# Optimization experiments

Measured on AMD Instinct MI355X. Metric: run time of the kernel, lower is better.

Reference implementation:

```python
import jax, jax.numpy as jnp
import numpy as np

D = 128      # d_model
H = 8        # n_heads
HD = D // H  # head_dim = 16
E = 256      # n_experts
R = 32       # kv_lora_rank
B, T = 4, 512
EPS = 1e-6


def _dense_init(k, fi, fo):
    s = float(1.0 / np.sqrt(fi))
    return jax.random.uniform(k, (fi, fo), minval=-s, maxval=s, dtype=jnp.float32)


def setup_inputs() -> dict:
    key = jax.random.key(0)
    ks = jax.random.split(key, 16)
    rng = np.random.RandomState(42)
    Q, _ = np.linalg.qr(rng.randn(D, D))
    glim = float(np.sqrt(6.0 / (D + D)))
    return {
        'x': jax.random.normal(ks[0], (B, T, D), dtype=jnp.float32),
        'g1': jnp.ones((D,), jnp.float32),
        'qW': _dense_init(ks[1], D, D), 'qb': jnp.zeros((D,), jnp.float32),
        'kdW': _dense_init(ks[2], D, R), 'kdb': jnp.zeros((R,), jnp.float32),
        'kuW': _dense_init(ks[3], R, 2 * D), 'kub': jnp.zeros((2 * D,), jnp.float32),
        'oW': _dense_init(ks[4], D, D), 'ob': jnp.zeros((D,), jnp.float32),
        'rot': jnp.asarray(Q, jnp.float32),
        'tq_scale': jnp.ones((D,), jnp.float32),
        's1W': _dense_init(ks[5], D, D), 's1b': jnp.zeros((D,), jnp.float32),
        's2W': _dense_init(ks[6], D, D), 's2b': jnp.zeros((D,), jnp.float32),
        'g2': jnp.ones((D,), jnp.float32),
        'gateW': _dense_init(ks[7], D, E), 'gateb': jnp.zeros((E,), jnp.float32),
        'expW': jax.random.uniform(ks[8], (E, D, D), minval=-glim, maxval=glim, dtype=jnp.float32),
        'm1W': _dense_init(ks[9], D, D), 'm1b': jnp.zeros((D,), jnp.float32),
        'm2W': _dense_init(ks[10], D, D), 'm2b': jnp.zeros((D,), jnp.float32),
    }


def _rmsnorm(x, g):
    return g * (x / jnp.sqrt(jnp.mean(x * x, axis=-1, keepdims=True) + EPS))


def _swiglu(x, w1, b1, w2, b2):
    gate = x @ w1 + b1
    return gate * jax.nn.sigmoid(gate) * (x @ w2 + b2)


def _mla(x, qW, qb, kdW, kdb, kuW, kub, oW, ob):
    b, t = x.shape[0], x.shape[1]
    q = (x @ qW + qb).reshape(b, t, H, HD)
    kv = ((x @ kdW + kdb) @ kuW + kub).reshape(b, t, H, 2 * HD)
    k, v = jnp.split(kv, 2, axis=-1)
    q = jax.nn.elu(q) + 1.0
    k = jax.nn.elu(k) + 1.0
    # linear attention: context[b,h,d,e] = sum_t k[b,t,h,d] v[b,t,h,e]
    context = jnp.einsum('bthd,bthe->bhde', k, v)
    out = jnp.einsum('bthd,bhde->bthe', q, context)
    k_sum = jnp.sum(k, axis=1)  # [b,h,d]
    z = 1.0 / (jnp.einsum('bthd,bhd->bth', q, k_sum) + EPS)
    out = out * z[..., None]
    return out.reshape(b, t, D) @ oW + ob


def _turbo_quant(x, rot, scale):
    x = x @ rot
    mag = jnp.sqrt(jnp.mean(x * x, axis=-1, keepdims=True) + EPS)
    phase = x / mag
    qp = jnp.clip(phase * 127.0, -127.0, 127.0) / 127.0
    phase = jax.lax.stop_gradient(qp - phase) + phase  # straight-through
    return phase * mag * scale


def _moe(h, gateW, gateb, expW, m1W, m1b, m2W, m2b):
    gate_scores = jax.nn.softmax(h @ gateW + gateb, axis=-1)  # [B,T,E]
    top_vals, top_idx = jax.lax.top_k(gate_scores, 2)
    top_w = top_vals / (jnp.sum(top_vals, axis=-1, keepdims=True) + EPS)
    # dense all-expert compute as in the original module
    eo = jnp.einsum('btd,edo->bteo', h, expW)  # [B,T,E,D]
    mask = jnp.sum(jax.nn.one_hot(top_idx, E, dtype=h.dtype) * top_w[..., None], axis=2)  # [B,T,E]
    wavg = jnp.einsum('bteo,bte->bto', eo, mask)
    wavg = _swiglu(wavg, m1W, m1b, m2W, m2b)
    diff_sq = jnp.square(eo - wavg[:, :, None, :])
    wvar = jnp.einsum('bteo,bte->bto', diff_sq, mask)
    consensus = jnp.exp(-jnp.mean(wvar, axis=-1))  # [B,T]
    return wavg, consensus


def reference(x, g1, qW, qb, kdW, kdb, kuW, kub, oW, ob, rot, tq_scale,
              s1W, s1b, s2W, s2b, g2, gateW, gateb, expW, m1W, m1b, m2W, m2b):
    attn_out = _turbo_quant(_mla(_rmsnorm(x, g1), qW, qb, kdW, kdb, kuW, kub, oW, ob), rot, tq_scale)
    x = x + _swiglu(attn_out, s1W, s1b, s2W, s2b)
    moe_out, consensus = _moe(_rmsnorm(x, g2), gateW, gateb, expW, m1W, m1b, m2W, m2b)
    return x + moe_out, consensus
```

## Files before the change

kernel.cpp:

```cpp
#include <hip/hip_runtime.h>
#include <hip/hip_bf16.h>
#include <math.h>

static constexpr int Dd   = 128;
static constexpr int NH   = 8;
static constexpr int HD   = 16;
static constexpr int NE   = 256;
static constexpr int RR   = 32;
static constexpr int BB   = 4;
static constexpr int TT   = 512;
static constexpr int NTOK = BB * TT;
static constexpr int TPB  = 4;
static constexpr int SLOTS = 256;
#define EPSF 1e-6f

__device__ __forceinline__ float elu1(float v) { return v > 0.f ? v + 1.f : expf(v); }
__device__ __forceinline__ float sigm(float v) { return 1.f / (1.f + expf(-v)); }

__global__ __launch_bounds__(256) void k_init(
    const float* __restrict__ oW, const float* __restrict__ ob,
    const float* __restrict__ rot,
    const float* __restrict__ kdW, const float* __restrict__ kdb,
    const float* __restrict__ kuW, const float* __restrict__ kub,
    float* __restrict__ oR, float* __restrict__ bR,
    float* __restrict__ kvW, float* __restrict__ bkv,
    float* __restrict__ ctx, float* __restrict__ ksum, int* __restrict__ cnt) {
  const int blk = blockIdx.x, tid = threadIdx.x;
  if (blk < 64) {
    int row = blk * 2 + (tid >> 7), col = tid & 127;
    const float* ow = oW + row * 128;
    float acc = 0.f;
#pragma unroll 8
    for (int k = 0; k < 128; k++) acc += ow[k] * rot[k * 128 + col];
    oR[row * 128 + col] = acc;
  } else if (blk == 64) {
    if (tid < 128) {
      float acc = 0.f;
#pragma unroll 8
      for (int k = 0; k < 128; k++) acc += ob[k] * rot[k * 128 + tid];
      bR[tid] = acc;
    }
    {
      float acc = kub[tid];
#pragma unroll
      for (int k = 0; k < 32; k++) acc += kdb[k] * kuW[k * 256 + tid];
      bkv[tid] = acc;
    }
    for (int i = tid; i < 32 * 256; i += 256) ctx[i] = 0.f;
    for (int i = tid; i < 512; i += 256) ksum[i] = 0.f;
    cnt[tid] = 0;
  } else {
    int idx = (blk - 65) * 256 + tid;
    int row = idx >> 8, col = idx & 255;
    const float* kw = kdW + row * 32;
    float acc = 0.f;
#pragma unroll
    for (int k = 0; k < 32; k++) acc += kw[k] * kuW[k * 256 + col];
    kvW[row * 256 + col] = acc;
  }
}

__global__ __launch_bounds__(768) void k_pre(
    const float* __restrict__ x, const float* __restrict__ g1,
    const float* __restrict__ qW, const float* __restrict__ qb,
    const float* __restrict__ kvW, const float* __restrict__ bkv,
    float* __restrict__ qbuf, float* __restrict__ kvbuf) {
  const int tid = threadIdx.x;
  const int lane = tid & 63;
  const int n0 = blockIdx.x * TPB;

  __shared__ float4 xgT[128];
  __shared__ float4 qpart[128];
  __shared__ float4 kvpart[256];
  __shared__ float4 rtmp[2];

  if (tid < 128) {
    int j = tid;
    float g1j = g1[j];
    float v[4], xg[4];
#pragma unroll
    for (int t = 0; t < 4; t++) {
      float xv = x[(n0 + t) * Dd + j];
      v[t] = xv * xv;
      xg[t] = xv * g1j;
    }
    xgT[j] = make_float4(xg[0], xg[1], xg[2], xg[3]);
#pragma unroll
    for (int o = 32; o > 0; o >>= 1) {
#pragma unroll
      for (int t = 0; t < 4; t++) v[t] += __shfl_xor(v[t], o, 64);
    }
    if (lane == 0) rtmp[tid >> 6] = make_float4(v[0], v[1], v[2], v[3]);
  }
  __syncthreads();

  float a0 = 0, a1 = 0, a2 = 0, a3 = 0;
  const bool isq = tid < 256;
  int j, kh;
  if (isq) {
    j = tid & 127; kh = tid >> 7;
    const float* Wp = qW + (kh * 64) * Dd + j;
    const float4* hb = xgT + kh * 64;
#pragma unroll 16
    for (int i = 0; i < 64; i++) {
      float4 h4 = hb[i];
      float w = Wp[i * Dd];
      a0 += h4.x * w; a1 += h4.y * w; a2 += h4.z * w; a3 += h4.w * w;
    }
    if (kh) qpart[j] = make_float4(a0, a1, a2, a3);
  } else {
    int u = tid - 256;
    j = u & 255; kh = u >> 8;
    const float* Wp = kvW + (kh * 64) * 256 + j;
    const float4* hb = xgT + kh * 64;
#pragma unroll 16
    for (int i = 0; i < 64; i++) {
      float4 h4 = hb[i];
      float w = Wp[i * 256];
      a0 += h4.x * w; a1 += h4.y * w; a2 += h4.z * w; a3 += h4.w * w;
    }
    if (kh) kvpart[j] = make_float4(a0, a1, a2, a3);
  }
  __syncthreads();

  if (kh == 0) {
    float r[4];
#pragma unroll
    for (int t = 0; t < 4; t++) {
      float ss = ((const float*)&rtmp[0])[t] + ((const float*)&rtmp[1])[t];
      r[t] = rsqrtf(ss * (1.f / 128.f) + EPSF);
    }
    if (isq) {
      float4 p = qpart[j];
      float bb = qb[j];
      qbuf[(n0 + 0) * Dd + j] = elu1((a0 + p.x) * r[0] + bb);
      qbuf[(n0 + 1) * Dd + j] = elu1((a1 + p.y) * r[1] + bb);
      qbuf[(n0 + 2) * Dd + j] = elu1((a2 + p.z) * r[2] + bb);
      qbuf[(n0 + 3) * Dd + j] = elu1((a3 + p.w) * r[3] + bb);
    } else {
      float4 p = kvpart[j];
      float bb = bkv[j];
      bool isk = (j & 31) < 16;
      float v0 = (a0 + p.x) * r[0] + bb, v1 = (a1 + p.y) * r[1] + bb;
      float v2 = (a2 + p.z) * r[2] + bb, v3 = (a3 + p.w) * r[3] + bb;
      kvbuf[(n0 + 0) * 256 + j] = isk ? elu1(v0) : v0;
      kvbuf[(n0 + 1) * 256 + j] = isk ? elu1(v1) : v1;
      kvbuf[(n0 + 2) * 256 + j] = isk ? elu1(v2) : v2;
      kvbuf[(n0 + 3) * 256 + j] = isk ? elu1(v3) : v3;
    }
  }
}

__global__ __launch_bounds__(256) void k_ctx(const float* __restrict__ kv,
                                             float* __restrict__ ctx,
                                             float* __restrict__ ksum) {
  const int blk = blockIdx.x;
  const int bh = blk >> 3, c = blk & 7;
  const int b = bh >> 3, h = bh & 7;
  const int tid = threadIdx.x;
  const int d = tid >> 4, e = tid & 15;
  __shared__ float sh[64 * 32];
#pragma unroll
  for (int r = 0; r < 8; r++) {
    int lin = r * 256 + tid;
    int tok = lin >> 5, off = lin & 31;
    sh[lin] = kv[((b * TT + c * 64 + tok) * 256) + h * 32 + off];
  }
  __syncthreads();
  float acc = 0.f, ks = 0.f;
#pragma unroll 4
  for (int t = 0; t < 64; t++) {
    float kk = sh[t * 32 + d];
    acc += kk * sh[t * 32 + 16 + e];
    ks += kk;
  }
  atomicAdd(&ctx[bh * 256 + d * 16 + e], acc);
  if (e == 0) atomicAdd(&ksum[bh * 16 + d], ks);
}

__global__ __launch_bounds__(512) void k_mid(
    const float* __restrict__ x, const float* __restrict__ qbuf,
    const float* __restrict__ ctx, const float* __restrict__ ksum,
    const float* __restrict__ oR, const float* __restrict__ bR,
    const float* __restrict__ tqs,
    const float* __restrict__ s1W, const float* __restrict__ s1b,
    const float* __restrict__ s2W, const float* __restrict__ s2b,
    const float* __restrict__ g2, const float* __restrict__ gateW,
    const float* __restrict__ gateb,
    float* __restrict__ xnbuf, float* __restrict__ h2buf,
    float* __restrict__ gw, int* __restrict__ tokslot,
    int* __restrict__ slottok, int* __restrict__ cnt) {
  const int tid = threadIdx.x;
  const int j = tid & 127, g = tid >> 7;
  const int lane = tid & 63;
  const int n0 = blockIdx.x * TPB;
  const int b = n0 >> 9;

  __shared__ float4 bufA[128], bufB[128];
  __shared__ float4 part[3][128];
  __shared__ float4 gpart[256];
  __shared__ float4 rtmp[2];
  __shared__ float wvS[4][4]; __shared__ int wiS[4][4];
  __shared__ float zS[4][4];

  float xres[4];
  if (tid < 128) {
#pragma unroll
    for (int t = 0; t < 4; t++) xres[t] = x[(n0 + t) * Dd + j];
  }

  ((float*)&bufA[j])[g] = qbuf[(n0 + g) * Dd + j];
  __syncthreads();

  if (tid < 128) {
    int h = j >> 4, e = j & 15;
    const float* cpt = ctx + (b * NH + h) * 256;
    const float* kpt = ksum + (b * NH + h) * 16;
    float num[4] = {0, 0, 0, 0}, den[4] = {0, 0, 0, 0};
#pragma unroll
    for (int d = 0; d < 16; d++) {
      float cx = cpt[d * 16 + e], ks = kpt[d];
      float4 q4 = bufA[h * 16 + d];
      num[0] += q4.x * cx; num[1] += q4.y * cx; num[2] += q4.z * cx; num[3] += q4.w * cx;
      den[0] += q4.x * ks; den[1] += q4.y * ks; den[2] += q4.z * ks; den[3] += q4.w * ks;
    }
#pragma unroll
    for (int t = 0; t < 4; t++) ((float*)&bufB[j])[t] = num[t] / (den[t] + EPSF);
  }
  __syncthreads();

  {
    float a0 = 0, a1 = 0, a2 = 0, a3 = 0;
    const float* Wp = oR + (g * 32) * Dd + j;
#pragma unroll 16
    for (int i = 0; i < 32; i++) {
      float4 h4 = bufB[g * 32 + i];
      float w = Wp[i * Dd];
      a0 += h4.x * w; a1 += h4.y * w; a2 += h4.z * w; a3 += h4.w * w;
    }
    if (g) part[g - 1][j] = make_float4(a0, a1, a2, a3);
    __syncthreads();
    float tot[4];
    if (g == 0) {
      float4 p0 = part[0][j], p1 = part[1][j], p2 = part[2][j];
      float bb = bR[j];
      tot[0] = a0 + p0.x + p1.x + p2.x + bb; tot[1] = a1 + p0.y + p1.y + p2.y + bb;
      tot[2] = a2 + p0.z + p1.z + p2.z + bb; tot[3] = a3 + p0.w + p1.w + p2.w + bb;
      float v[4];
#pragma unroll
      for (int t = 0; t < 4; t++) v[t] = tot[t] * tot[t];
#pragma unroll
      for (int o = 32; o > 0; o >>= 1) {
#pragma unroll
        for (int t = 0; t < 4; t++) v[t] += __shfl_xor(v[t], o, 64);
      }
      if (lane == 0) rtmp[tid >> 6] = make_float4(v[0], v[1], v[2], v[3]);
    }
    __syncthreads();
    if (g == 0) {
      float scj = tqs[j];
#pragma unroll
      for (int t = 0; t < 4; t++) {
        float ss = ((const float*)&rtmp[0])[t] + ((const float*)&rtmp[1])[t];
        float mag = sqrtf(ss * (1.f / 128.f) + EPSF);
        float zc = fminf(fmaxf(tot[t], -mag), mag);
        ((float*)&bufA[j])[t] = zc * scj;
      }
    }
    __syncthreads();
  }

  {
    float a0 = 0, a1 = 0, a2 = 0, a3 = 0;
    const float* Wp = (g < 2 ? s1W : s2W) + ((g & 1) * 64) * Dd + j;
#pragma unroll 16
    for (int i = 0; i < 64; i++) {
      float4 h4 = bufA[(g & 1) * 64 + i];
      float w = Wp[i * Dd];
      a0 += h4.x * w; a1 += h4.y * w; a2 += h4.z * w; a3 += h4.w * w;
    }
    if (g) part[g - 1][j] = make_float4(a0, a1, a2, a3);
    __syncthreads();
    if (g == 0) {
      float b1 = s1b[j], b2 = s2b[j];
      float4 p0 = part[0][j], p1 = part[1][j], p2 = part[2][j];
      float gv[4], uv[4], xn[4], v[4];
      gv[0] = a0 + p0.x + b1; gv[1] = a1 + p0.y + b1;
      gv[2] = a2 + p0.z + b1; gv[3] = a3 + p0.w + b1;
      uv[0] = p1.x + p2.x + b2; uv[1] = p1.y + p2.y + b2;
      uv[2] = p1.z + p2.z + b2; uv[3] = p1.w + p2.w + b2;
      float g2j = g2[j];
#pragma unroll
      for (int t = 0; t < 4; t++) {
        xn[t] = xres[t] + gv[t] * sigm(gv[t]) * uv[t];
        xnbuf[(n0 + t) * Dd + j] = xn[t];
        ((float*)&bufB[j])[t] = g2j * xn[t];
        v[t] = xn[t] * xn[t];
      }
#pragma unroll
      for (int o = 32; o > 0; o >>= 1) {
#pragma unroll
        for (int t = 0; t < 4; t++) v[t] += __shfl_xor(v[t], o, 64);
      }
      if (lane == 0) rtmp[tid >> 6] = make_float4(v[0], v[1], v[2], v[3]);
    }
    __syncthreads();
  }

  float val[4];
  float r2[4];
  {
    int col = tid & 255, kh = tid >> 8;
    float a0 = 0, a1 = 0, a2 = 0, a3 = 0;
    const float* Wp = gateW + (kh * 64) * NE + col;
#pragma unroll 16
    for (int i = 0; i < 64; i++) {
      float4 h4 = bufB[kh * 64 + i];
      float w = Wp[i * NE];
      a0 += h4.x * w; a1 += h4.y * w; a2 += h4.z * w; a3 += h4.w * w;
    }
    if (kh) gpart[col] = make_float4(a0, a1, a2, a3);
    __syncthreads();
#pragma unroll
    for (int t = 0; t < 4; t++) {
      float ss = ((const float*)&rtmp[0])[t] + ((const float*)&rtmp[1])[t];
      r2[t] = rsqrtf(ss * (1.f / 128.f) + EPSF);
    }
    if (!kh) {
      float4 p = gpart[col];
      float bb = gateb[col];
      val[0] = (a0 + p.x) * r2[0] + bb; val[1] = (a1 + p.y) * r2[1] + bb;
      val[2] = (a2 + p.z) * r2[2] + bb; val[3] = (a3 + p.w) * r2[3] + bb;
    }
    if (tid < 128) {
#pragma unroll
      for (int t = 0; t < 4; t++)
        h2buf[(n0 + t) * Dd + j] = ((const float*)&bufB[j])[t] * r2[t];
    }
  }
  __syncthreads();

  float m1[4]; int i1[4];
  {
    if (tid < 256) {
      float bv[4]; int bi[4];
#pragma unroll
      for (int t = 0; t < 4; t++) { bv[t] = val[t]; bi[t] = tid; }
#pragma unroll
      for (int o = 32; o > 0; o >>= 1) {
#pragma unroll
        for (int t = 0; t < 4; t++) {
          float wv = __shfl_xor(bv[t], o, 64);
          int wi = __shfl_xor(bi[t], o, 64);
          if (wv > bv[t] || (wv == bv[t] && wi < bi[t])) { bv[t] = wv; bi[t] = wi; }
        }
      }
      if (lane == 0) {
#pragma unroll
        for (int t = 0; t < 4; t++) { wvS[tid >> 6][t] = bv[t]; wiS[tid >> 6][t] = bi[t]; }
      }
    }
    __syncthreads();
    if (tid < 256) {
#pragma unroll
      for (int t = 0; t < 4; t++) {
        m1[t] = wvS[0][t]; i1[t] = wiS[0][t];
#pragma unroll
        for (int w = 1; w < 4; w++) {
          float cv = wvS[w][t]; int ci = wiS[w][t];
          if (cv > m1[t] || (cv == m1[t] && ci < i1[t])) { m1[t] = cv; i1[t] = ci; }
        }
      }
    }
    __syncthreads();
  }
  float m2[4]; int i2[4];
  {
    if (tid < 256) {
      float bv[4]; int bi[4];
#pragma unroll
      for (int t = 0; t < 4; t++) {
        bv[t] = (tid == i1[t]) ? -INFINITY : val[t];
        bi[t] = tid;
      }
#pragma unroll
      for (int o = 32; o > 0; o >>= 1) {
#pragma unroll
        for (int t = 0; t < 4; t++) {
          float wv = __shfl_xor(bv[t], o, 64);
          int wi = __shfl_xor(bi[t], o, 64);
          if (wv > bv[t] || (wv == bv[t] && wi < bi[t])) { bv[t] = wv; bi[t] = wi; }
        }
      }
      if (lane == 0) {
#pragma unroll
        for (int t = 0; t < 4; t++) { wvS[tid >> 6][t] = bv[t]; wiS[tid >> 6][t] = bi[t]; }
      }
    }
    __syncthreads();
    if (tid < 256) {
#pragma unroll
      for (int t = 0; t < 4; t++) {
        m2[t] = wvS[0][t]; i2[t] = wiS[0][t];
#pragma unroll
        for (int w = 1; w < 4; w++) {
          float cv = wvS[w][t]; int ci = wiS[w][t];
          if (cv > m2[t] || (cv == m2[t] && ci < i2[t])) { m2[t] = cv; i2[t] = ci; }
        }
      }
    }
    __syncthreads();
  }
  {
    if (tid < 256) {
      float v[4];
#pragma unroll
      for (int t = 0; t < 4; t++) v[t] = expf(val[t] - m1[t]);
#pragma unroll
      for (int o = 32; o > 0; o >>= 1) {
#pragma unroll
        for (int t = 0; t < 4; t++) v[t] += __shfl_xor(v[t], o, 64);
      }
      if (lane == 0) {
#pragma unroll
        for (int t = 0; t < 4; t++) zS[tid >> 6][t] = v[t];
      }
    }
    __syncthreads();
  }
  if (tid < 4) {
    int t = tid, tok = n0 + t;
    float Z = zS[0][t] + zS[1][t] + zS[2][t] + zS[3][t];
    float p1 = 1.f / Z;
    float p2 = expf(m2[t] - m1[t]) / Z;
    float s = p1 + p2 + EPSF;
    int e1 = i1[t], e2 = i2[t];
    int s1 = atomicAdd(&cnt[e1], 1); if (s1 > SLOTS - 1) s1 = SLOTS - 1;
    int s2 = atomicAdd(&cnt[e2], 1); if (s2 > SLOTS - 1) s2 = SLOTS - 1;
    int sl1 = e1 * SLOTS + s1, sl2 = e2 * SLOTS + s2;
    slottok[sl1] = tok; slottok[sl2] = tok;
    tokslot[tok * 2] = sl1; tokslot[tok * 2 + 1] = sl2;
    gw[tok * 2] = p1 / s; gw[tok * 2 + 1] = p2 / s;
  }
}

__global__ __launch_bounds__(512) void k_exp(const float* __restrict__ h2buf,
                                             const int* __restrict__ slottok,
                                             const int* __restrict__ cnt,
                                             const float* __restrict__ expW,
                                             float* __restrict__ ybuf) {
  const int e = blockIdx.x;
  int n = cnt[e]; if (n > SLOTS) n = SLOTS;
  if (n == 0) return;
  const int base = e * SLOTS;
  const int tid = threadIdx.x;
  const int j = tid & 127, g = tid >> 7;
  __shared__ __align__(16) float hT[128 * 20];
  const float* Wp = expW + (size_t)e * Dd * Dd + j;
  for (int t0 = 0; t0 < n; t0 += 16) {
    int m = n - t0; if (m > 16) m = 16;
    __syncthreads();
    for (int tt = g; tt < m; tt += 4) {
      int tok = slottok[base + t0 + tt];
      hT[j * 20 + tt] = h2buf[tok * Dd + j];
    }
    __syncthreads();
    float acc[4] = {0, 0, 0, 0};
#pragma unroll 8
    for (int i = 0; i < 128; i++) {
      float w = Wp[i * Dd];
      float4 h4 = *(const float4*)&hT[i * 20 + g * 4];
      acc[0] += h4.x * w; acc[1] += h4.y * w; acc[2] += h4.z * w; acc[3] += h4.w * w;
    }
#pragma unroll
    for (int k = 0; k < 4; k++) {
      int tt = g * 4 + k;
      if (tt < m) ybuf[(size_t)(base + t0 + tt) * Dd + j] = acc[k];
    }
  }
}

__global__ __launch_bounds__(512) void k_post(
    const float* __restrict__ xnbuf, const float* __restrict__ ybuf,
    const int* __restrict__ tokslot, const float* __restrict__ gw,
    const float* __restrict__ m1W, const float* __restrict__ m1b,
    const float* __restrict__ m2W, const float* __restrict__ m2b,
    float* __restrict__ out) {
  const int tid = threadIdx.x;
  const int j = tid & 127, g = tid >> 7;
  const int lane = tid & 63;
  const int n0 = blockIdx.x * TPB;

  __shared__ float4 y1T[128], y2T[128], inT[128], sT[128];
  __shared__ float4 part[3][128];
  __shared__ float4 rtmp[2];
  __shared__ int sSlot[4][2];
  __shared__ float sWt[4][2];

  if (tid < 4) {
    sSlot[tid][0] = tokslot[(n0 + tid) * 2];
    sSlot[tid][1] = tokslot[(n0 + tid) * 2 + 1];
    sWt[tid][0] = gw[(n0 + tid) * 2];
    sWt[tid][1] = gw[(n0 + tid) * 2 + 1];
  }
  __syncthreads();

  {
    float y1 = ybuf[(size_t)sSlot[g][0] * Dd + j];
    float y2 = ybuf[(size_t)sSlot[g][1] * Dd + j];
    ((float*)&y1T[j])[g] = y1;
    ((float*)&y2T[j])[g] = y2;
    ((float*)&inT[j])[g] = sWt[g][0] * y1 + sWt[g][1] * y2;
  }
  __syncthreads();

  {
    float a0 = 0, a1 = 0, a2 = 0, a3 = 0;
    const float* Wp = (g < 2 ? m1W : m2W) + ((g & 1) * 64) * Dd + j;
#pragma unroll 16
    for (int i = 0; i < 64; i++) {
      float4 h4 = inT[(g & 1) * 64 + i];
      float w = Wp[i * Dd];
      a0 += h4.x * w; a1 += h4.y * w; a2 += h4.z * w; a3 += h4.w * w;
    }
    if (g) part[g - 1][j] = make_float4(a0, a1, a2, a3);
    __syncthreads();
    if (g == 0) {
      float b1 = m1b[j], b2 = m2b[j];
      float4 p0 = part[0][j], p1 = part[1][j], p2 = part[2][j];
      float gv[4], uv[4];
      gv[0] = a0 + p0.x + b1; gv[1] = a1 + p0.y + b1;
      gv[2] = a2 + p0.z + b1; gv[3] = a3 + p0.w + b1;
      uv[0] = p1.x + p2.x + b2; uv[1] = p1.y + p2.y + b2;
      uv[2] = p1.z + p2.z + b2; uv[3] = p1.w + p2.w + b2;
#pragma unroll
      for (int t = 0; t < 4; t++) {
        float sv = gv[t] * sigm(gv[t]) * uv[t];
        ((float*)&sT[j])[t] = sv;
        out[(n0 + t) * Dd + j] = xnbuf[(n0 + t) * Dd + j] + sv;
      }
    }
    __syncthreads();
  }

  if (tid < 128) {
    float v[4];
#pragma unroll
    for (int t = 0; t < 4; t++) {
      float sv = ((const float*)&sT[j])[t];
      float d1 = ((const float*)&y1T[j])[t] - sv;
      float d2 = ((const float*)&y2T[j])[t] - sv;
      v[t] = sWt[t][0] * d1 * d1 + sWt[t][1] * d2 * d2;
    }
#pragma unroll
    for (int o = 32; o > 0; o >>= 1) {
#pragma unroll
      for (int t = 0; t < 4; t++) v[t] += __shfl_xor(v[t], o, 64);
    }
    if (lane == 0) rtmp[tid >> 6] = make_float4(v[0], v[1], v[2], v[3]);
  }
  __syncthreads();
  if (tid < 4) {
    float s = ((const float*)&rtmp[0])[tid] + ((const float*)&rtmp[1])[tid];
    out[NTOK * Dd + n0 + tid] = expf(-s * (1.f / 128.f));
  }
}

extern "C" void kernel_launch(void* const* d_in, const int* in_sizes, int n_in,
                              void* d_out, int out_size, void* d_ws, size_t ws_size,
                              hipStream_t stream) {
  const float* x   = (const float*)d_in[0];
  const float* g1  = (const float*)d_in[1];
  const float* qW  = (const float*)d_in[2];
  const float* qb  = (const float*)d_in[3];
  const float* kdW = (const float*)d_in[4];
  const float* kdb = (const float*)d_in[5];
  const float* kuW = (const float*)d_in[6];
  const float* kub = (const float*)d_in[7];
  const float* oW  = (const float*)d_in[8];
  const float* ob  = (const float*)d_in[9];
  const float* rot = (const float*)d_in[10];
  const float* tqs = (const float*)d_in[11];
  const float* s1W = (const float*)d_in[12];
  const float* s1b = (const float*)d_in[13];
  const float* s2W = (const float*)d_in[14];
  const float* s2b = (const float*)d_in[15];
  const float* g2  = (const float*)d_in[16];
  const float* gW  = (const float*)d_in[17];
  const float* gb  = (const float*)d_in[18];
  const float* eW  = (const float*)d_in[19];
  const float* m1W = (const float*)d_in[20];
  const float* m1b = (const float*)d_in[21];
  const float* m2W = (const float*)d_in[22];
  const float* m2b = (const float*)d_in[23];
  float* out = (float*)d_out;
  float* ws  = (float*)d_ws;

  float* qbuf   = ws;
  float* kvbuf  = ws + 262144;
  float* ctx    = ws + 786432;
  float* ksum   = ws + 794624;
  float* h2buf  = ws + 795136;
  float* xnbuf  = ws + 1057280;
  float* gw     = ws + 1319424;
  float* oRb    = ws + 1323520;
  float* bRb    = ws + 1339904;
  float* kvW    = ws + 1340032;
  float* bkv    = ws + 1372800;
  int*   cnt     = (int*)(ws + 1373056);
  int*   tokslot = (int*)(ws + 1373312);
  int*   slottok = (int*)(ws + 1377408);
  float* ybuf   = ws + 1442944;

  k_init<<<193, 256, 0, stream>>>(oW, ob, rot, kdW, kdb, kuW, kub,
                                  oRb, bRb, kvW, bkv, ctx, ksum, cnt);
  k_pre<<<NTOK / TPB, 768, 0, stream>>>(x, g1, qW, qb, kvW, bkv, qbuf, kvbuf);
  k_ctx<<<256, 256, 0, stream>>>(kvbuf, ctx, ksum);
  k_mid<<<NTOK / TPB, 512, 0, stream>>>(x, qbuf, ctx, ksum, oRb, bRb, tqs,
                                        s1W, s1b, s2W, s2b, g2, gW, gb,
                                        xnbuf, h2buf, gw, tokslot, slottok, cnt);
  k_exp<<<NE, 512, 0, stream>>>(h2buf, slottok, cnt, eW, ybuf);
  k_post<<<NTOK / TPB, 512, 0, stream>>>(xnbuf, ybuf, tokslot, gw,
                                         m1W, m1b, m2W, m2b, out);
}
```

Measured before the change: 168.5 us.

## Fuse all stages into one cooperative persistent kernel with grid syncs

Replaces the six separate kernel launches with a single cooperative kernel of 256 blocks that separates the stages with grid-wide syncs. Each block now handles 8 tokens instead of 4, and q and the residual stay in shared memory instead of round-tripping through global buffers. The goal is to remove launch gaps and intermediate global traffic. In exchange, each stage runs on only 256 blocks (lower occupancy than the earlier 512-block launches), grid-sync barriers add cost, and per-thread register pressure rises.

New measurement: 333.1 us. +97.7%, slower.

```diff
diff --git a/kernel.cpp b/kernel.cpp
--- a/kernel.cpp
+++ b/kernel.cpp
@@ -1,56 +1,76 @@
 #include <hip/hip_runtime.h>
-#include <hip/hip_bf16.h>
+#include <hip/hip_cooperative_groups.h>
 #include <math.h>
+
+namespace cg = cooperative_groups;
 
 static constexpr int Dd   = 128;
 static constexpr int NH   = 8;
-static constexpr int HD   = 16;
 static constexpr int NE   = 256;
-static constexpr int RR   = 32;
-static constexpr int BB   = 4;
 static constexpr int TT   = 512;
-static constexpr int NTOK = BB * TT;
-static constexpr int TPB  = 4;
+static constexpr int NTOK = 2048;
 static constexpr int SLOTS = 256;
 #define EPSF 1e-6f
 
 __device__ __forceinline__ float elu1(float v) { return v > 0.f ? v + 1.f : expf(v); }
 __device__ __forceinline__ float sigm(float v) { return 1.f / (1.f + expf(-v)); }
 
-__global__ __launch_bounds__(256) void k_init(
-    const float* __restrict__ oW, const float* __restrict__ ob,
-    const float* __restrict__ rot,
+__global__ __launch_bounds__(512, 2) void k_all(
+    const float* __restrict__ x, const float* __restrict__ g1,
+    const float* __restrict__ qW, const float* __restrict__ qb,
     const float* __restrict__ kdW, const float* __restrict__ kdb,
     const float* __restrict__ kuW, const float* __restrict__ kub,
-    float* __restrict__ oR, float* __restrict__ bR,
+    const float* __restrict__ oW, const float* __restrict__ ob,
+    const float* __restrict__ rot, const float* __restrict__ tqs,
+    const float* __restrict__ s1W, const float* __restrict__ s1b,
+    const float* __restrict__ s2W, const float* __restrict__ s2b,
+    const float* __restrict__ g2, const float* __restrict__ gateW,
+    const float* __restrict__ gateb, const float* __restrict__ expW,
+    const float* __restrict__ m1W, const float* __restrict__ m1b,
+    const float* __restrict__ m2W, const float* __restrict__ m2b,
+    float* __restrict__ kvbuf, float* __restrict__ ctx, float* __restrict__ ksum,
+    float* __restrict__ h2buf, float* __restrict__ oR, float* __restrict__ bR,
     float* __restrict__ kvW, float* __restrict__ bkv,
-    float* __restrict__ ctx, float* __restrict__ ksum, int* __restrict__ cnt) {
+    int* __restrict__ cnt, int* __restrict__ slottok,
+    float* __restrict__ ybuf, float* __restrict__ out) {
+  cg::grid_group grid = cg::this_grid();
   const int blk = blockIdx.x, tid = threadIdx.x;
-  if (blk < 64) {
-    int row = blk * 2 + (tid >> 7), col = tid & 127;
+  const int lane = tid & 63;
+  const int n0 = blk * 8;
+
+  __shared__ __align__(16) float sm[9232];
+  float* qT  = sm + 7184;
+  float* xnT = sm + 8208;
+  __shared__ float wvS[4][8]; __shared__ int wiS[4][8]; __shared__ float zS[4][8];
+  __shared__ float sWt[8][2]; __shared__ int sSlot[8][2];
+
+  if (blk < 32) {
+    int idx = blk * 512 + tid;
+    int row = idx >> 7, col = idx & 127;
     const float* ow = oW + row * 128;
     float acc = 0.f;
 #pragma unroll 8
     for (int k = 0; k < 128; k++) acc += ow[k] * rot[k * 128 + col];
     oR[row * 128 + col] = acc;
-  } else if (blk == 64) {
+  } else if (blk == 32) {
     if (tid < 128) {
       float acc = 0.f;
 #pragma unroll 8
       for (int k = 0; k < 128; k++) acc += ob[k] * rot[k * 128 + tid];
       bR[tid] = acc;
     }
-    {
+    if (tid < 256) {
       float acc = kub[tid];
 #pragma unroll
       for (int k = 0; k < 32; k++) acc += kdb[k] * kuW[k * 256 + tid];
       bkv[tid] = acc;
     }
-    for (int i = tid; i < 32 * 256; i += 256) ctx[i] = 0.f;
-    for (int i = tid; i < 512; i += 256) ksum[i] = 0.f;
-    cnt[tid] = 0;
-  } else {
-    int idx = (blk - 65) * 256 + tid;
+  } else if (blk == 33) {
+    for (int i = tid; i < 32 * 256; i += 512) ctx[i] = 0.f;
+    ksum[tid] = 0.f;
+    if (tid < 256) cnt[tid] = 0;
+  } else if (blk >= 34 && blk < 98) {
+    int idx = (blk - 34) * 512 + tid;
     int row = idx >> 8, col = idx & 255;
     const float* kw = kdW + row * 32;
     float acc = 0.f;
@@ -58,298 +78,277 @@
     for (int k = 0; k < 32; k++) acc += kw[k] * kuW[k * 256 + col];
     kvW[row * 256 + col] = acc;
   }
-}
-
-__global__ __launch_bounds__(768) void k_pre(
-    const float* __restrict__ x, const float* __restrict__ g1,
-    const float* __restrict__ qW, const float* __restrict__ qb,
-    const float* __restrict__ kvW, const float* __restrict__ bkv,
-    float* __restrict__ qbuf, float* __restrict__ kvbuf) {
-  const int tid = threadIdx.x;
-  const int lane = tid & 63;
-  const int n0 = blockIdx.x * TPB;
-
-  __shared__ float4 xgT[128];
-  __shared__ float4 qpart[128];
-  __shared__ float4 kvpart[256];
-  __shared__ float4 rtmp[2];
-
-  if (tid < 128) {
-    int j = tid;
-    float g1j = g1[j];
-    float v[4], xg[4];
-#pragma unroll
-    for (int t = 0; t < 4; t++) {
-      float xv = x[(n0 + t) * Dd + j];
-      v[t] = xv * xv;
-      xg[t] = xv * g1j;
-    }
-    xgT[j] = make_float4(xg[0], xg[1], xg[2], xg[3]);
-#pragma unroll
-    for (int o = 32; o > 0; o >>= 1) {
-#pragma unroll
-      for (int t = 0; t < 4; t++) v[t] += __shfl_xor(v[t], o, 64);
-    }
-    if (lane == 0) rtmp[tid >> 6] = make_float4(v[0], v[1], v[2], v[3]);
+  grid.sync();
+
+  {
+    float* xgT   = sm;
+    float* qpart = sm + 1024;
+    float* rtmp  = sm + 2048;
+    if (tid < 128) {
+      float g1j = g1[tid];
+      float v[8];
+#pragma unroll
+      for (int t = 0; t < 8; t++) {
+        float xv = x[(n0 + t) * Dd + tid];
+        v[t] = xv * xv;
+        xgT[tid * 8 + t] = xv * g1j;
+      }
+#pragma unroll
+      for (int o = 32; o > 0; o >>= 1) {
+#pragma unroll
+        for (int t = 0; t < 8; t++) v[t] += __shfl_xor(v[t], o, 64);
+      }
+      if (lane == 0) {
+#pragma unroll
+        for (int t = 0; t < 8; t++) rtmp[(tid >> 6) * 8 + t] = v[t];
+      }
+    }
+    __syncthreads();
+
+    float acc[8] = {0, 0, 0, 0, 0, 0, 0, 0};
+    if (tid < 256) {
+      int j = tid & 127, kh = tid >> 7;
+      const float* Wp = qW + (kh * 64) * Dd + j;
+      const float* hb = xgT + (kh * 64) * 8;
+#pragma unroll 8
+      for (int i = 0; i < 64; i++) {
+        float w = Wp[i * Dd];
+        float4 A = *(const float4*)(hb + i * 8);
+        float4 B = *(const float4*)(hb + i * 8 + 4);
+        acc[0] += A.x * w; acc[1] += A.y * w; acc[2] += A.z * w; acc[3] += A.w * w;
+        acc[4] += B.x * w; acc[5] += B.y * w; acc[6] += B.z * w; acc[7] += B.w * w;
+      }
+      if (kh) {
+        *(float4*)(qpart + j * 8)     = make_float4(acc[0], acc[1], acc[2], acc[3]);
+        *(float4*)(qpart + j * 8 + 4) = make_float4(acc[4], acc[5], acc[6], acc[7]);
+      }
+    } else {
+      int col = tid - 256;
+      const float* Wp = kvW + col;
+#pragma unroll 8
+      for (int i = 0; i < 128; i++) {
+        float w = Wp[i * 256];
+        float4 A = *(const float4*)(xgT + i * 8);
+        float4 B = *(const float4*)(xgT + i * 8 + 4);
+        acc[0] += A.x * w; acc[1] += A.y * w; acc[2] += A.z * w; acc[3] += A.w * w;
+        acc[4] += B.x * w; acc[5] += B.y * w; acc[6] += B.z * w; acc[7] += B.w * w;
+      }
+    }
+    __syncthreads();
+
+    float r[8];
+#pragma unroll
+    for (int t = 0; t < 8; t++)
+      r[t] = rsqrtf((rtmp[t] + rtmp[8 + t]) * (1.f / 128.f) + EPSF);
+    if (tid < 128) {
+      float bb = qb[tid];
+#pragma unroll
+      for (int t = 0; t < 8; t++)
+        qT[tid * 8 + t] = elu1((acc[t] + qpart[tid * 8 + t]) * r[t] + bb);
+    } else if (tid >= 256) {
+      int col = tid - 256;
+      float bb = bkv[col];
+      bool isk = (col & 31) < 16;
+#pragma unroll
+      for (int t = 0; t < 8; t++) {
+        float v = acc[t] * r[t] + bb;
+        kvbuf[(n0 + t) * 256 + col] = isk ? elu1(v) : v;
+      }
+    }
   }
-  __syncthreads();
-
-  float a0 = 0, a1 = 0, a2 = 0, a3 = 0;
-  const bool isq = tid < 256;
-  int j, kh;
-  if (isq) {
-    j = tid & 127; kh = tid >> 7;
-    const float* Wp = qW + (kh * 64) * Dd + j;
-    const float4* hb = xgT + kh * 64;
-#pragma unroll 16
-    for (int i = 0; i < 64; i++) {
-      float4 h4 = hb[i];
-      float w = Wp[i * Dd];
-      a0 += h4.x * w; a1 += h4.y * w; a2 += h4.z * w; a3 += h4.w * w;
-    }
-    if (kh) qpart[j] = make_float4(a0, a1, a2, a3);
-  } else {
-    int u = tid - 256;
-    j = u & 255; kh = u >> 8;
-    const float* Wp = kvW + (kh * 64) * 256 + j;
-    const float4* hb = xgT + kh * 64;
-#pragma unroll 16
-    for (int i = 0; i < 64; i++) {
-      float4 h4 = hb[i];
-      float w = Wp[i * 256];
-      a0 += h4.x * w; a1 += h4.y * w; a2 += h4.z * w; a3 += h4.w * w;
-    }
-    if (kh) kvpart[j] = make_float4(a0, a1, a2, a3);
+  grid.sync();
+
+  {
+    float* sh = sm;
+    int bh = blk >> 3, c = blk & 7;
+    int b = bh >> 3, h = bh & 7;
+#pragma unroll
+    for (int r = 0; r < 4; r++) {
+      int lin = r * 512 + tid;
+      int tok = lin >> 5, off = lin & 31;
+      sh[lin] = kvbuf[((b * TT + c * 64 + tok) * 256) + h * 32 + off];
+    }
+    __syncthreads();
+    if (tid < 256) {
+      int d = tid >> 4, e = tid & 15;
+      float acc = 0.f, ks = 0.f;
+#pragma unroll 4
+      for (int t = 0; t < 64; t++) {
+        float kk = sh[t * 32 + d];
+        acc += kk * sh[t * 32 + 16 + e];
+        ks += kk;
+      }
+      atomicAdd(&ctx[bh * 256 + d * 16 + e], acc);
+      if (e == 0) atomicAdd(&ksum[bh * 16 + d], ks);
+    }
   }
-  __syncthreads();
-
-  if (kh == 0) {
-    float r[4];
-#pragma unroll
-    for (int t = 0; t < 4; t++) {
-      float ss = ((const float*)&rtmp[0])[t] + ((const float*)&rtmp[1])[t];
-      r[t] = rsqrtf(ss * (1.f / 128.f) + EPSF);
-    }
-    if (isq) {
-      float4 p = qpart[j];
-      float bb = qb[j];
-      qbuf[(n0 + 0) * Dd + j] = elu1((a0 + p.x) * r[0] + bb);
-      qbuf[(n0 + 1) * Dd + j] = elu1((a1 + p.y) * r[1] + bb);
-      qbuf[(n0 + 2) * Dd + j] = elu1((a2 + p.z) * r[2] + bb);
-      qbuf[(n0 + 3) * Dd + j] = elu1((a3 + p.w) * r[3] + bb);
-    } else {
-      float4 p = kvpart[j];
-      float bb = bkv[j];
-      bool isk = (j & 31) < 16;
-      float v0 = (a0 + p.x) * r[0] + bb, v1 = (a1 + p.y) * r[1] + bb;
-      float v2 = (a2 + p.z) * r[2] + bb, v3 = (a3 + p.w) * r[3] + bb;
-      kvbuf[(n0 + 0) * 256 + j] = isk ? elu1(v0) : v0;
-      kvbuf[(n0 + 1) * 256 + j] = isk ? elu1(v1) : v1;
-      kvbuf[(n0 + 2) * 256 + j] = isk ? elu1(v2) : v2;
-      kvbuf[(n0 + 3) * 256 + j] = isk ? elu1(v3) : v3;
-    }
-  }
-}
-
-__global__ __launch_bounds__(256) void k_ctx(const float* __restrict__ kv,
-                                             float* __restrict__ ctx,
-                                             float* __restrict__ ksum) {
-  const int blk = blockIdx.x;
-  const int bh = blk >> 3, c = blk & 7;
-  const int b = bh >> 3, h = bh & 7;
-  const int tid = threadIdx.x;
-  const int d = tid >> 4, e = tid & 15;
-  __shared__ float sh[64 * 32];
-#pragma unroll
-  for (int r = 0; r < 8; r++) {
-    int lin = r * 256 + tid;
-    int tok = lin >> 5, off = lin & 31;
-    sh[lin] = kv[((b * TT + c * 64 + tok) * 256) + h * 32 + off];
-  }
-  __syncthreads();
-  float acc = 0.f, ks = 0.f;
-#pragma unroll 4
-  for (int t = 0; t < 64; t++) {
-    float kk = sh[t * 32 + d];
-    acc += kk * sh[t * 32 + 16 + e];
-    ks += kk;
-  }
-  atomicAdd(&ctx[bh * 256 + d * 16 + e], acc);
-  if (e == 0) atomicAdd(&ksum[bh * 16 + d], ks);
-}
-
-__global__ __launch_bounds__(512) void k_mid(
-    const float* __restrict__ x, const float* __restrict__ qbuf,
-    const float* __restrict__ ctx, const float* __restrict__ ksum,
-    const float* __restrict__ oR, const float* __restrict__ bR,
-    const float* __restrict__ tqs,
-    const float* __restrict__ s1W, const float* __restrict__ s1b,
-    const float* __restrict__ s2W, const float* __restrict__ s2b,
-    const float* __restrict__ g2, const float* __restrict__ gateW,
-    const float* __restrict__ gateb,
-    float* __restrict__ xnbuf, float* __restrict__ h2buf,
-    float* __restrict__ gw, int* __restrict__ tokslot,
-    int* __restrict__ slottok, int* __restrict__ cnt) {
-  const int tid = threadIdx.x;
-  const int j = tid & 127, g = tid >> 7;
-  const int lane = tid & 63;
-  const int n0 = blockIdx.x * TPB;
-  const int b = n0 >> 9;
-
-  __shared__ float4 bufA[128], bufB[128];
-  __shared__ float4 part[3][128];
-  __shared__ float4 gpart[256];
-  __shared__ float4 rtmp[2];
-  __shared__ float wvS[4][4]; __shared__ int wiS[4][4];
-  __shared__ float zS[4][4];
-
-  float xres[4];
-  if (tid < 128) {
-#pragma unroll
-    for (int t = 0; t < 4; t++) xres[t] = x[(n0 + t) * Dd + j];
-  }
-
-  ((float*)&bufA[j])[g] = qbuf[(n0 + g) * Dd + j];
-  __syncthreads();
-
-  if (tid < 128) {
-    int h = j >> 4, e = j & 15;
-    const float* cpt = ctx + (b * NH + h) * 256;
-    const float* kpt = ksum + (b * NH + h) * 16;
-    float num[4] = {0, 0, 0, 0}, den[4] = {0, 0, 0, 0};
-#pragma unroll
-    for (int d = 0; d < 16; d++) {
-      float cx = cpt[d * 16 + e], ks = kpt[d];
-      float4 q4 = bufA[h * 16 + d];
-      num[0] += q4.x * cx; num[1] += q4.y * cx; num[2] += q4.z * cx; num[3] += q4.w * cx;
-      den[0] += q4.x * ks; den[1] += q4.y * ks; den[2] += q4.z * ks; den[3] += q4.w * ks;
-    }
-#pragma unroll
-    for (int t = 0; t < 4; t++) ((float*)&bufB[j])[t] = num[t] / (den[t] + EPSF);
-  }
-  __syncthreads();
+  grid.sync();
 
   {
-    float a0 = 0, a1 = 0, a2 = 0, a3 = 0;
-    const float* Wp = oR + (g * 32) * Dd + j;
-#pragma unroll 16
-    for (int i = 0; i < 32; i++) {
-      float4 h4 = bufB[g * 32 + i];
-      float w = Wp[i * Dd];
-      a0 += h4.x * w; a1 += h4.y * w; a2 += h4.z * w; a3 += h4.w * w;
-    }
-    if (g) part[g - 1][j] = make_float4(a0, a1, a2, a3);
-    __syncthreads();
-    float tot[4];
-    if (g == 0) {
-      float4 p0 = part[0][j], p1 = part[1][j], p2 = part[2][j];
-      float bb = bR[j];
-      tot[0] = a0 + p0.x + p1.x + p2.x + bb; tot[1] = a1 + p0.y + p1.y + p2.y + bb;
-      tot[2] = a2 + p0.z + p1.z + p2.z + bb; tot[3] = a3 + p0.w + p1.w + p2.w + bb;
-      float v[4];
-#pragma unroll
-      for (int t = 0; t < 4; t++) v[t] = tot[t] * tot[t];
+    float* bufA  = sm;
+    float* bufB  = sm + 1024;
+    float* part  = sm + 2048;
+    float* gpart = sm + 5120;
+    float* rtmp  = sm + 7168;
+    const int j = tid & 127, g = tid >> 7;
+
+    float xres[8];
+    if (tid < 128) {
+#pragma unroll
+      for (int t = 0; t < 8; t++) xres[t] = x[(n0 + t) * Dd + j];
+    }
+    if (tid < 128) {
+      int h = j >> 4, e = j & 15;
+      const float* cpt = ctx + ((n0 >> 9) * NH + h) * 256;
+      const float* kpt = ksum + ((n0 >> 9) * NH + h) * 16;
+      float num[8] = {0, 0, 0, 0, 0, 0, 0, 0}, den[8] = {0, 0, 0, 0, 0, 0, 0, 0};
+#pragma unroll
+      for (int d = 0; d < 16; d++) {
+        float cx = cpt[d * 16 + e], ks = kpt[d];
+        const float* q8 = qT + (h * 16 + d) * 8;
+#pragma unroll
+        for (int t = 0; t < 8; t++) { float qd = q8[t]; num[t] += qd * cx; den[t] += qd * ks; }
+      }
+#pragma unroll
+      for (int t = 0; t < 8; t++) bufB[j * 8 + t] = num[t] / (den[t] + EPSF);
+    }
+    __syncthreads();
+
+    {
+      float acc[8] = {0, 0, 0, 0, 0, 0, 0, 0};
+      const float* Wp = oR + (g * 32) * Dd + j;
+      const float* hb = bufB + (g * 32) * 8;
+#pragma unroll 8
+      for (int i = 0; i < 32; i++) {
+        float w = Wp[i * Dd];
+        float4 A = *(const float4*)(hb + i * 8);
+        float4 B = *(const float4*)(hb + i * 8 + 4);
+        acc[0] += A.x * w; acc[1] += A.y * w; acc[2] += A.z * w; acc[3] += A.w * w;
+        acc[4] += B.x * w; acc[5] += B.y * w; acc[6] += B.z * w; acc[7] += B.w * w;
+      }
+      if (g) {
+        *(float4*)(part + (g - 1) * 1024 + j * 8)     = make_float4(acc[0], acc[1], acc[2], acc[3]);
+        *(float4*)(part + (g - 1) * 1024 + j * 8 + 4) = make_float4(acc[4], acc[5], acc[6], acc[7]);
+      }
+      __syncthreads();
+      float tot[8];
+      if (g == 0) {
+        float bb = bR[j];
+        float v[8];
+#pragma unroll
+        for (int t = 0; t < 8; t++) {
+          tot[t] = acc[t] + part[j * 8 + t] + part[1024 + j * 8 + t] + part[2048 + j * 8 + t] + bb;
+          v[t] = tot[t] * tot[t];
+        }
+#pragma unroll
+        for (int o = 32; o > 0; o >>= 1) {
+#pragma unroll
+          for (int t = 0; t < 8; t++) v[t] += __shfl_xor(v[t], o, 64);
+        }
+        if (lane == 0) {
+#pragma unroll
+          for (int t = 0; t < 8; t++) rtmp[(tid >> 6) * 8 + t] = v[t];
+        }
+      }
+      __syncthreads();
+      if (g == 0) {
+        float scj = tqs[j];
+#pragma unroll
+        for (int t = 0; t < 8; t++) {
+          float mag = sqrtf((rtmp[t] + rtmp[8 + t]) * (1.f / 128.f) + EPSF);
+          float zc = fminf(fmaxf(tot[t], -mag), mag);
+          bufA[j * 8 + t] = zc * scj;
+        }
+      }
+      __syncthreads();
+    }
+
+    {
+      float acc[8] = {0, 0, 0, 0, 0, 0, 0, 0};
+      const float* Wp = (g < 2 ? s1W : s2W) + ((g & 1) * 64) * Dd + j;
+      const float* hb = bufA + ((g & 1) * 64) * 8;
+#pragma unroll 8
+      for (int i = 0; i < 64; i++) {
+        float w = Wp[i * Dd];
+        float4 A = *(const float4*)(hb + i * 8);
+        float4 B = *(const float4*)(hb + i * 8 + 4);
+        acc[0] += A.x * w; acc[1] += A.y * w; acc[2] += A.z * w; acc[3] += A.w * w;
+        acc[4] += B.x * w; acc[5] += B.y * w; acc[6] += B.z * w; acc[7] += B.w * w;
+      }
+      if (g) {
+        *(float4*)(part + (g - 1) * 1024 + j * 8)     = make_float4(acc[0], acc[1], acc[2], acc[3]);
+        *(float4*)(part + (g - 1) * 1024 + j * 8 + 4) = make_float4(acc[4], acc[5], acc[6], acc[7]);
+      }
+      __syncthreads();
+      if (g == 0) {
+        float b1 = s1b[j], b2 = s2b[j], g2j = g2[j];
+        float v[8];
+#pragma unroll
+        for (int t = 0; t < 8; t++) {
+          float gv = acc[t] + part[j * 8 + t] + b1;
+          float uv = part[1024 + j * 8 + t] + part[2048 + j * 8 + t] + b2;
+          float xn = xres[t] + gv * sigm(gv) * uv;
+          xnT[j * 8 + t] = xn;
+          bufB[j * 8 + t] = g2j * xn;
+          v[t] = xn * xn;
+        }
+#pragma unroll
+        for (int o = 32; o > 0; o >>= 1) {
+#pragma unroll
+          for (int t = 0; t < 8; t++) v[t] += __shfl_xor(v[t], o, 64);
+        }
+        if (lane == 0) {
+#pragma unroll
+          for (int t = 0; t < 8; t++) rtmp[(tid >> 6) * 8 + t] = v[t];
+        }
+      }
+      __syncthreads();
+    }
+
+    float val[8], r2[8];
+    {
+      int col = tid & 255, kh = tid >> 8;
+      float acc[8] = {0, 0, 0, 0, 0, 0, 0, 0};
+      const float* Wp = gateW + (kh * 64) * NE + col;
+      const float* hb = bufB + (kh * 64) * 8;
+#pragma unroll 8
+      for (int i = 0; i < 64; i++) {
+        float w = Wp[i * NE];
+        float4 A = *(const float4*)(hb + i * 8);
+        float4 B = *(const float4*)(hb + i * 8 + 4);
+        acc[0] += A.x * w; acc[1] += A.y * w; acc[2] += A.z * w; acc[3] += A.w * w;
+        acc[4] += B.x * w; acc[5] += B.y * w; acc[6] += B.z * w; acc[7] += B.w * w;
+      }
+      if (kh) {
+        *(float4*)(gpart + col * 8)     = make_float4(acc[0], acc[1], acc[2], acc[3]);
+        *(float4*)(gpart + col * 8 + 4) = make_float4(acc[4], acc[5], acc[6], acc[7]);
+      }
+      __syncthreads();
+#pragma unroll
+      for (int t = 0; t < 8; t++)
+        r2[t] = rsqrtf((rtmp[t] + rtmp[8 + t]) * (1.f / 128.f) + EPSF);
+      if (!kh) {
+        float bb = gateb[col];
+#pragma unroll
+        for (int t = 0; t < 8; t++) val[t] = (acc[t] + gpart[col * 8 + t]) * r2[t] + bb;
+      }
+      if (tid < 128) {
+#pragma unroll
+        for (int t = 0; t < 8; t++)
+          h2buf[(n0 + t) * Dd + j] = bufB[j * 8 + t] * r2[t];
+      }
+    }
+    __syncthreads();
+
+    float m1[8]; int i1[8];
+    if (tid < 256) {
+      float bv[8]; int bi[8];
+#pragma unroll
+      for (int t = 0; t < 8; t++) { bv[t] = val[t]; bi[t] = tid; }
 #pragma unroll
       for (int o = 32; o > 0; o >>= 1) {
 #pragma unroll
-        for (int t = 0; t < 4; t++) v[t] += __shfl_xor(v[t], o, 64);
-      }
-      if (lane == 0) rtmp[tid >> 6] = make_float4(v[0], v[1], v[2], v[3]);
-    }
-    __syncthreads();
-    if (g == 0) {
-      float scj = tqs[j];
-#pragma unroll
-      for (int t = 0; t < 4; t++) {
-        float ss = ((const float*)&rtmp[0])[t] + ((const float*)&rtmp[1])[t];
-        float mag = sqrtf(ss * (1.f / 128.f) + EPSF);
-        float zc = fminf(fmaxf(tot[t], -mag), mag);
-        ((float*)&bufA[j])[t] = zc * scj;
-      }
-    }
-    __syncthreads();
-  }
-
-  {
-    float a0 = 0, a1 = 0, a2 = 0, a3 = 0;
-    const float* Wp = (g < 2 ? s1W : s2W) + ((g & 1) * 64) * Dd + j;
-#pragma unroll 16
-    for (int i = 0; i < 64; i++) {
-      float4 h4 = bufA[(g & 1) * 64 + i];
-      float w = Wp[i * Dd];
-      a0 += h4.x * w; a1 += h4.y * w; a2 += h4.z * w; a3 += h4.w * w;
-    }
-    if (g) part[g - 1][j] = make_float4(a0, a1, a2, a3);
-    __syncthreads();
-    if (g == 0) {
-      float b1 = s1b[j], b2 = s2b[j];
-      float4 p0 = part[0][j], p1 = part[1][j], p2 = part[2][j];
-      float gv[4], uv[4], xn[4], v[4];
-      gv[0] = a0 + p0.x + b1; gv[1] = a1 + p0.y + b1;
-      gv[2] = a2 + p0.z + b1; gv[3] = a3 + p0.w + b1;
-      uv[0] = p1.x + p2.x + b2; uv[1] = p1.y + p2.y + b2;
-      uv[2] = p1.z + p2.z + b2; uv[3] = p1.w + p2.w + b2;
-      float g2j = g2[j];
-#pragma unroll
-      for (int t = 0; t < 4; t++) {
-        xn[t] = xres[t] + gv[t] * sigm(gv[t]) * uv[t];
-        xnbuf[(n0 + t) * Dd + j] = xn[t];
-        ((float*)&bufB[j])[t] = g2j * xn[t];
-        v[t] = xn[t] * xn[t];
-      }
-#pragma unroll
-      for (int o = 32; o > 0; o >>= 1) {
-#pragma unroll
-        for (int t = 0; t < 4; t++) v[t] += __shfl_xor(v[t], o, 64);
-      }
-      if (lane == 0) rtmp[tid >> 6] = make_float4(v[0], v[1], v[2], v[3]);
-    }
-    __syncthreads();
-  }
-
-  float val[4];
-  float r2[4];
-  {
-    int col = tid & 255, kh = tid >> 8;
-    float a0 = 0, a1 = 0, a2 = 0, a3 = 0;
-    const float* Wp = gateW + (kh * 64) * NE + col;
-#pragma unroll 16
-    for (int i = 0; i < 64; i++) {
-      float4 h4 = bufB[kh * 64 + i];
-      float w = Wp[i * NE];
-      a0 += h4.x * w; a1 += h4.y * w; a2 += h4.z * w; a3 += h4.w * w;
-    }
-    if (kh) gpart[col] = make_float4(a0, a1, a2, a3);
-    __syncthreads();
-#pragma unroll
-    for (int t = 0; t < 4; t++) {
-      float ss = ((const float*)&rtmp[0])[t] + ((const float*)&rtmp[1])[t];
-      r2[t] = rsqrtf(ss * (1.f / 128.f) + EPSF);
-    }
-    if (!kh) {
-      float4 p = gpart[col];
-      float bb = gateb[col];
-      val[0] = (a0 + p.x) * r2[0] + bb; val[1] = (a1 + p.y) * r2[1] + bb;
-      val[2] = (a2 + p.z) * r2[2] + bb; val[3] = (a3 + p.w) * r2[3] + bb;
-    }
-    if (tid < 128) {
-#pragma unroll
-      for (int t = 0; t < 4; t++)
-        h2buf[(n0 + t) * Dd + j] = ((const float*)&bufB[j])[t] * r2[t];
-    }
-  }
-  __syncthreads();
-
-  float m1[4]; int i1[4];
-  {
-    if (tid < 256) {
-      float bv[4]; int bi[4];
-#pragma unroll
-      for (int t = 0; t < 4; t++) { bv[t] = val[t]; bi[t] = tid; }
-#pragma unroll
-      for (int o = 32; o > 0; o >>= 1) {
-#pragma unroll
-        for (int t = 0; t < 4; t++) {
+        for (int t = 0; t < 8; t++) {
           float wv = __shfl_xor(bv[t], o, 64);
           int wi = __shfl_xor(bi[t], o, 64);
           if (wv > bv[t] || (wv == bv[t] && wi < bi[t])) { bv[t] = wv; bi[t] = wi; }
@@ -357,13 +356,13 @@
       }
       if (lane == 0) {
 #pragma unroll
-        for (int t = 0; t < 4; t++) { wvS[tid >> 6][t] = bv[t]; wiS[tid >> 6][t] = bi[t]; }
-      }
-    }
-    __syncthreads();
-    if (tid < 256) {
-#pragma unroll
-      for (int t = 0; t < 4; t++) {
+        for (int t = 0; t < 8; t++) { wvS[tid >> 6][t] = bv[t]; wiS[tid >> 6][t] = bi[t]; }
+      }
+    }
+    __syncthreads();
+    if (tid < 256) {
+#pragma unroll
+      for (int t = 0; t < 8; t++) {
         m1[t] = wvS[0][t]; i1[t] = wiS[0][t];
 #pragma unroll
         for (int w = 1; w < 4; w++) {
@@ -373,20 +372,18 @@
       }
     }
     __syncthreads();
-  }
-  float m2[4]; int i2[4];
-  {
-    if (tid < 256) {
-      float bv[4]; int bi[4];
-#pragma unroll
-      for (int t = 0; t < 4; t++) {
+    float m2[8]; int i2[8];
+    if (tid < 256) {
+      float bv[8]; int bi[8];
+#pragma unroll
+      for (int t = 0; t < 8; t++) {
         bv[t] = (tid == i1[t]) ? -INFINITY : val[t];
         bi[t] = tid;
       }
 #pragma unroll
       for (int o = 32; o > 0; o >>= 1) {
 #pragma unroll
-        for (int t = 0; t < 4; t++) {
+        for (int t = 0; t < 8; t++) {
           float wv = __shfl_xor(bv[t], o, 64);
           int wi = __shfl_xor(bi[t], o, 64);
           if (wv > bv[t] || (wv == bv[t] && wi < bi[t])) { bv[t] = wv; bi[t] = wi; }
@@ -394,13 +391,13 @@
       }
       if (lane == 0) {
 #pragma unroll
-        for (int t = 0; t < 4; t++) { wvS[tid >> 6][t] = bv[t]; wiS[tid >> 6][t] = bi[t]; }
-      }
-    }
-    __syncthreads();
-    if (tid < 256) {
-#pragma unroll
-      for (int t = 0; t < 4; t++) {
+        for (int t = 0; t < 8; t++) { wvS[tid >> 6][t] = bv[t]; wiS[tid >> 6][t] = bi[t]; }
+      }
+    }
+    __syncthreads();
+    if (tid < 256) {
+#pragma unroll
+      for (int t = 0; t < 8; t++) {
         m2[t] = wvS[0][t]; i2[t] = wiS[0][t];
 #pragma unroll
         for (int w = 1; w < 4; w++) {
@@ -410,159 +407,144 @@
       }
     }
     __syncthreads();
+    if (tid < 256) {
+      float v[8];
+#pragma unroll
+      for (int t = 0; t < 8; t++) v[t] = expf(val[t] - m1[t]);
+#pragma unroll
+      for (int o = 32; o > 0; o >>= 1) {
+#pragma unroll
+        for (int t = 0; t < 8; t++) v[t] += __shfl_xor(v[t], o, 64);
+      }
+      if (lane == 0) {
+#pragma unroll
+        for (int t = 0; t < 8; t++) zS[tid >> 6][t] = v[t];
+      }
+    }
+    __syncthreads();
+    if (tid < 8) {
+      int t = tid, tok = n0 + t;
+      float Z = zS[0][t] + zS[1][t] + zS[2][t] + zS[3][t];
+      float p1 = 1.f / Z;
+      float p2 = expf(m2[t] - m1[t]) / Z;
+      float s = p1 + p2 + EPSF;
+      int e1 = i1[t], e2 = i2[t];
+      int s1 = atomicAdd(&cnt[e1], 1); if (s1 > SLOTS - 1) s1 = SLOTS - 1;
+      int s2 = atomicAdd(&cnt[e2], 1); if (s2 > SLOTS - 1) s2 = SLOTS - 1;
+      int sl1 = e1 * SLOTS + s1, sl2 = e2 * SLOTS + s2;
+      slottok[sl1] = tok; slottok[sl2] = tok;
+      sSlot[t][0] = sl1; sSlot[t][1] = sl2;
+      sWt[t][0] = p1 / s; sWt[t][1] = p2 / s;
+    }
   }
+  grid.sync();
+
   {
-    if (tid < 256) {
-      float v[4];
-#pragma unroll
-      for (int t = 0; t < 4; t++) v[t] = expf(val[t] - m1[t]);
+    int e = blk;
+    int n = cnt[e]; if (n > SLOTS) n = SLOTS;
+    int base = e * SLOTS;
+    const int j = tid & 127, g = tid >> 7;
+    float* hT = sm;
+    const float* Wp = expW + (size_t)e * Dd * Dd + j;
+    for (int t0 = 0; t0 < n; t0 += 16) {
+      int m = n - t0; if (m > 16) m = 16;
+      __syncthreads();
+      for (int tt = g; tt < m; tt += 4) {
+        int tok = slottok[base + t0 + tt];
+        hT[j * 20 + tt] = h2buf[tok * Dd + j];
+      }
+      __syncthreads();
+      float acc[4] = {0, 0, 0, 0};
+#pragma unroll 8
+      for (int i = 0; i < 128; i++) {
+        float w = Wp[i * Dd];
+        float4 h4 = *(const float4*)&hT[i * 20 + g * 4];
+        acc[0] += h4.x * w; acc[1] += h4.y * w; acc[2] += h4.z * w; acc[3] += h4.w * w;
+      }
+#pragma unroll
+      for (int k = 0; k < 4; k++) {
+        int tt = g * 4 + k;
+        if (tt < m) ybuf[(size_t)(base + t0 + tt) * Dd + j] = acc[k];
+      }
+    }
+  }
+  grid.sync();
+
+  {
+    float* y1T  = sm;
+    float* y2T  = sm + 1024;
+    float* inT  = sm + 2048;
+    float* sT   = sm + 3072;
+    float* part = sm + 4096;
+    float* rtmp = sm + 7168;
+    const int j = tid & 127, g = tid >> 7;
+
+#pragma unroll
+    for (int tt = 0; tt < 2; tt++) {
+      int t = g * 2 + tt;
+      float y1 = ybuf[(size_t)sSlot[t][0] * Dd + j];
+      float y2 = ybuf[(size_t)sSlot[t][1] * Dd + j];
+      y1T[j * 8 + t] = y1;
+      y2T[j * 8 + t] = y2;
+      inT[j * 8 + t] = sWt[t][0] * y1 + sWt[t][1] * y2;
+    }
+    __syncthreads();
+
+    {
+      float acc[8] = {0, 0, 0, 0, 0, 0, 0, 0};
+      const float* Wp = (g < 2 ? m1W : m2W) + ((g & 1) * 64) * Dd + j;
+      const float* hb = inT + ((g & 1) * 64) * 8;
+#pragma unroll 8
+      for (int i = 0; i < 64; i++) {
+        float w = Wp[i * Dd];
+        float4 A = *(const float4*)(hb + i * 8);
+        float4 B = *(const float4*)(hb + i * 8 + 4);
+        acc[0] += A.x * w; acc[1] += A.y * w; acc[2] += A.z * w; acc[3] += A.w * w;
+        acc[4] += B.x * w; acc[5] += B.y * w; acc[6] += B.z * w; acc[7] += B.w * w;
+      }
+      if (g) {
+        *(float4*)(part + (g - 1) * 1024 + j * 8)     = make_float4(acc[0], acc[1], acc[2], acc[3]);
+        *(float4*)(part + (g - 1) * 1024 + j * 8 + 4) = make_float4(acc[4], acc[5], acc[6], acc[7]);
+      }
+      __syncthreads();
+      if (g == 0) {
+        float b1 = m1b[j], b2 = m2b[j];
+#pragma unroll
+        for (int t = 0; t < 8; t++) {
+          float gv = acc[t] + part[j * 8 + t] + b1;
+          float uv = part[1024 + j * 8 + t] + part[2048 + j * 8 + t] + b2;
+          float sv = gv * sigm(gv) * uv;
+          sT[j * 8 + t] = sv;
+          out[(n0 + t) * Dd + j] = xnT[j * 8 + t] + sv;
+        }
+      }
+      __syncthreads();
+    }
+
+    if (tid < 128) {
+      float v[8];
+#pragma unroll
+      for (int t = 0; t < 8; t++) {
+        float sv = sT[j * 8 + t];
+        float d1 = y1T[j * 8 + t] - sv;
+        float d2 = y2T[j * 8 + t] - sv;
+        v[t] = sWt[t][0] * d1 * d1 + sWt[t][1] * d2 * d2;
+      }
 #pragma unroll
       for (int o = 32; o > 0; o >>= 1) {
 #pragma unroll
-        for (int t = 0; t < 4; t++) v[t] += __shfl_xor(v[t], o, 64);
+        for (int t = 0; t < 8; t++) v[t] += __shfl_xor(v[t], o, 64);
       }
       if (lane == 0) {
 #pragma unroll
-        for (int t = 0; t < 4; t++) zS[tid >> 6][t] = v[t];
-      }
-    }
-    __syncthreads();
-  }
-  if (tid < 4) {
-    int t = tid, tok = n0 + t;
-    float Z = zS[0][t] + zS[1][t] + zS[2][t] + zS[3][t];
-    float p1 = 1.f / Z;
-    float p2 = expf(m2[t] - m1[t]) / Z;
-    float s = p1 + p2 + EPSF;
-    int e1 = i1[t], e2 = i2[t];
-    int s1 = atomicAdd(&cnt[e1], 1); if (s1 > SLOTS - 1) s1 = SLOTS - 1;
-    int s2 = atomicAdd(&cnt[e2], 1); if (s2 > SLOTS - 1) s2 = SLOTS - 1;
-    int sl1 = e1 * SLOTS + s1, sl2 = e2 * SLOTS + s2;
-    slottok[sl1] = tok; slottok[sl2] = tok;
-    tokslot[tok * 2] = sl1; tokslot[tok * 2 + 1] = sl2;
-    gw[tok * 2] = p1 / s; gw[tok * 2 + 1] = p2 / s;
-  }
-}
-
-__global__ __launch_bounds__(512) void k_exp(const float* __restrict__ h2buf,
-                                             const int* __restrict__ slottok,
-                                             const int* __restrict__ cnt,
-                                             const float* __restrict__ expW,
-                                             float* __restrict__ ybuf) {
-  const int e = blockIdx.x;
-  int n = cnt[e]; if (n > SLOTS) n = SLOTS;
-  if (n == 0) return;
-  const int base = e * SLOTS;
-  const int tid = threadIdx.x;
-  const int j = tid & 127, g = tid >> 7;
-  __shared__ __align__(16) float hT[128 * 20];
-  const float* Wp = expW + (size_t)e * Dd * Dd + j;
-  for (int t0 = 0; t0 < n; t0 += 16) {
-    int m = n - t0; if (m > 16) m = 16;
-    __syncthreads();
-    for (int tt = g; tt < m; tt += 4) {
-      int tok = slottok[base + t0 + tt];
-      hT[j * 20 + tt] = h2buf[tok * Dd + j];
-    }
-    __syncthreads();
-    float acc[4] = {0, 0, 0, 0};
-#pragma unroll 8
-    for (int i = 0; i < 128; i++) {
-      float w = Wp[i * Dd];
-      float4 h4 = *(const float4*)&hT[i * 20 + g * 4];
-      acc[0] += h4.x * w; acc[1] += h4.y * w; acc[2] += h4.z * w; acc[3] += h4.w * w;
-    }
-#pragma unroll
-    for (int k = 0; k < 4; k++) {
-      int tt = g * 4 + k;
-      if (tt < m) ybuf[(size_t)(base + t0 + tt) * Dd + j] = acc[k];
-    }
-  }
-}
-
-__global__ __launch_bounds__(512) void k_post(
-    const float* __restrict__ xnbuf, const float* __restrict__ ybuf,
-    const int* __restrict__ tokslot, const float* __restrict__ gw,
-    const float* __restrict__ m1W, const float* __restrict__ m1b,
-    const float* __restrict__ m2W, const float* __restrict__ m2b,
-    float* __restrict__ out) {
-  const int tid = threadIdx.x;
-  const int j = tid & 127, g = tid >> 7;
-  const int lane = tid & 63;
-  const int n0 = blockIdx.x * TPB;
-
-  __shared__ float4 y1T[128], y2T[128], inT[128], sT[128];
-  __shared__ float4 part[3][128];
-  __shared__ float4 rtmp[2];
-  __shared__ int sSlot[4][2];
-  __shared__ float sWt[4][2];
-
-  if (tid < 4) {
-    sSlot[tid][0] = tokslot[(n0 + tid) * 2];
-    sSlot[tid][1] = tokslot[(n0 + tid) * 2 + 1];
-    sWt[tid][0] = gw[(n0 + tid) * 2];
-    sWt[tid][1] = gw[(n0 + tid) * 2 + 1];
-  }
-  __syncthreads();
-
-  {
-    float y1 = ybuf[(size_t)sSlot[g][0] * Dd + j];
-    float y2 = ybuf[(size_t)sSlot[g][1] * Dd + j];
-    ((float*)&y1T[j])[g] = y1;
-    ((float*)&y2T[j])[g] = y2;
-    ((float*)&inT[j])[g] = sWt[g][0] * y1 + sWt[g][1] * y2;
-  }
-  __syncthreads();
-
-  {
-    float a0 = 0, a1 = 0, a2 = 0, a3 = 0;
-    const float* Wp = (g < 2 ? m1W : m2W) + ((g & 1) * 64) * Dd + j;
-#pragma unroll 16
-    for (int i = 0; i < 64; i++) {
-      float4 h4 = inT[(g & 1) * 64 + i];
-      float w = Wp[i * Dd];
-      a0 += h4.x * w; a1 += h4.y * w; a2 += h4.z * w; a3 += h4.w * w;
-    }
-    if (g) part[g - 1][j] = make_float4(a0, a1, a2, a3);
-    __syncthreads();
-    if (g == 0) {
-      float b1 = m1b[j], b2 = m2b[j];
-      float4 p0 = part[0][j], p1 = part[1][j], p2 = part[2][j];
-      float gv[4], uv[4];
-      gv[0] = a0 + p0.x + b1; gv[1] = a1 + p0.y + b1;
-      gv[2] = a2 + p0.z + b1; gv[3] = a3 + p0.w + b1;
-      uv[0] = p1.x + p2.x + b2; uv[1] = p1.y + p2.y + b2;
-      uv[2] = p1.z + p2.z + b2; uv[3] = p1.w + p2.w + b2;
-#pragma unroll
-      for (int t = 0; t < 4; t++) {
-        float sv = gv[t] * sigm(gv[t]) * uv[t];
-        ((float*)&sT[j])[t] = sv;
-        out[(n0 + t) * Dd + j] = xnbuf[(n0 + t) * Dd + j] + sv;
-      }
-    }
-    __syncthreads();
-  }
-
-  if (tid < 128) {
-    float v[4];
-#pragma unroll
-    for (int t = 0; t < 4; t++) {
-      float sv = ((const float*)&sT[j])[t];
-      float d1 = ((const float*)&y1T[j])[t] - sv;
-      float d2 = ((const float*)&y2T[j])[t] - sv;
-      v[t] = sWt[t][0] * d1 * d1 + sWt[t][1] * d2 * d2;
-    }
-#pragma unroll
-    for (int o = 32; o > 0; o >>= 1) {
-#pragma unroll
-      for (int t = 0; t < 4; t++) v[t] += __shfl_xor(v[t], o, 64);
-    }
-    if (lane == 0) rtmp[tid >> 6] = make_float4(v[0], v[1], v[2], v[3]);
-  }
-  __syncthreads();
-  if (tid < 4) {
-    float s = ((const float*)&rtmp[0])[tid] + ((const float*)&rtmp[1])[tid];
-    out[NTOK * Dd + n0 + tid] = expf(-s * (1.f / 128.f));
+        for (int t = 0; t < 8; t++) rtmp[(tid >> 6) * 8 + t] = v[t];
+      }
+    }
+    __syncthreads();
+    if (tid < 8) {
+      float s = rtmp[tid] + rtmp[8 + tid];
+      out[NTOK * Dd + n0 + tid] = expf(-s * (1.f / 128.f));
+    }
   }
 }
 
@@ -596,30 +578,26 @@
   float* out = (float*)d_out;
   float* ws  = (float*)d_ws;
 
-  float* qbuf   = ws;
-  float* kvbuf  = ws + 262144;
-  float* ctx    = ws + 786432;
-  float* ksum   = ws + 794624;
-  float* h2buf  = ws + 795136;
-  float* xnbuf  = ws + 1057280;
-  float* gw     = ws + 1319424;
-  float* oRb    = ws + 1323520;
-  float* bRb    = ws + 1339904;
-  float* kvW    = ws + 1340032;
-  float* bkv    = ws + 1372800;
-  int*   cnt     = (int*)(ws + 1373056);
-  int*   tokslot = (int*)(ws + 1373312);
-  int*   slottok = (int*)(ws + 1377408);
-  float* ybuf   = ws + 1442944;
-
-  k_init<<<193, 256, 0, stream>>>(oW, ob, rot, kdW, kdb, kuW, kub,
-                                  oRb, bRb, kvW, bkv, ctx, ksum, cnt);
-  k_pre<<<NTOK / TPB, 768, 0, stream>>>(x, g1, qW, qb, kvW, bkv, qbuf, kvbuf);
-  k_ctx<<<256, 256, 0, stream>>>(kvbuf, ctx, ksum);
-  k_mid<<<NTOK / TPB, 512, 0, stream>>>(x, qbuf, ctx, ksum, oRb, bRb, tqs,
-                                        s1W, s1b, s2W, s2b, g2, gW, gb,
-                                        xnbuf, h2buf, gw, tokslot, slottok, cnt);
-  k_exp<<<NE, 512, 0, stream>>>(h2buf, slottok, cnt, eW, ybuf);
-  k_post<<<NTOK / TPB, 512, 0, stream>>>(xnbuf, ybuf, tokslot, gw,
-                                         m1W, m1b, m2W, m2b, out);
+  float* kvbuf   = ws;
+  float* ctx     = ws + 524288;
+  float* ksum    = ws + 532480;
+  float* h2buf   = ws + 532992;
+  float* oRb     = ws + 795136;
+  float* bRb     = ws + 811520;
+  float* kvW     = ws + 811648;
+  float* bkv     = ws + 844416;
+  int*   cnt     = (int*)(ws + 844672);
+  int*   slottok = (int*)(ws + 844928);
+  float* ybuf    = ws + 910464;
+
+  void* args[] = {
+    (void*)&x, (void*)&g1, (void*)&qW, (void*)&qb, (void*)&kdW, (void*)&kdb,
+    (void*)&kuW, (void*)&kub, (void*)&oW, (void*)&ob, (void*)&rot, (void*)&tqs,
+    (void*)&s1W, (void*)&s1b, (void*)&s2W, (void*)&s2b, (void*)&g2, (void*)&gW,
+    (void*)&gb, (void*)&eW, (void*)&m1W, (void*)&m1b, (void*)&m2W, (void*)&m2b,
+    (void*)&kvbuf, (void*)&ctx, (void*)&ksum, (void*)&h2buf, (void*)&oRb,
+    (void*)&bRb, (void*)&kvW, (void*)&bkv, (void*)&cnt, (void*)&slottok,
+    (void*)&ybuf, (void*)&out
+  };
+  hipLaunchCooperativeKernel((const void*)k_all, dim3(256), dim3(512), args, 0, stream);
 }
```
